# Performance work log

Measured on AMD Instinct MI355X. Metric: run time of the kernel, lower is better.

Reference implementation:

```python
import jax, jax.numpy as jnp
import numpy as np

HIDDEN = 512
HEADS = 8
D_HEAD = HIDDEN // HEADS
SCALE = D_HEAD ** -0.5
LN_EPS = 1e-5
N_L = 2048
N_R = 4096


def setup_inputs() -> dict:
    key = jax.random.key(0)
    ks = jax.random.split(key, 10)
    s = HIDDEN ** -0.5
    return {
        "q": jax.random.normal(ks[0], (N_L, HIDDEN), jnp.float32),
        "kv": jax.random.normal(ks[1], (N_R, HIDDEN), jnp.float32),
        "bias": jax.random.normal(ks[2], (N_L, N_R), jnp.float32),
        "Wq": jax.random.normal(ks[3], (HIDDEN, HIDDEN), jnp.float32) * s,
        "Wk": jax.random.normal(ks[4], (HIDDEN, HIDDEN), jnp.float32) * s,
        "Wv": jax.random.normal(ks[5], (HIDDEN, HIDDEN), jnp.float32) * s,
        "Wo": jax.random.normal(ks[6], (HIDDEN, HIDDEN), jnp.float32) * s,
        "bo": jnp.zeros((HIDDEN,), jnp.float32),
        "gamma": jnp.ones((HIDDEN,), jnp.float32),
        "beta": jnp.zeros((HIDDEN,), jnp.float32),
    }


def reference(q, kv, bias, Wq, Wk, Wv, Wo, bo, gamma, beta):
    # projections (torch Linear: x @ W.T)
    Q = (q @ Wq.T).reshape(N_L, HEADS, D_HEAD).transpose(1, 0, 2)   # [h, N_L, d]
    K = (kv @ Wk.T).reshape(N_R, HEADS, D_HEAD).transpose(1, 0, 2)  # [h, N_R, d]
    V = (kv @ Wv.T).reshape(N_R, HEADS, D_HEAD).transpose(1, 0, 2)  # [h, N_R, d]
    logits = SCALE * jnp.einsum('hld,hrd->hlr', Q, K) + bias[None]  # [h, N_L, N_R]
    attn = jax.nn.softmax(logits, axis=-1)                          # dropout p=0 -> identity
    ctx = jnp.einsum('hlr,hrd->hld', attn, V)                       # [h, N_L, d]
    ctx = ctx.transpose(1, 0, 2).reshape(N_L, HIDDEN)
    out = ctx @ Wo.T + bo
    x = out + q
    mu = jnp.mean(x, axis=-1, keepdims=True)
    var = jnp.mean((x - mu) ** 2, axis=-1, keepdims=True)
    out = (x - mu) * jax.lax.rsqrt(var + LN_EPS) * gamma + beta
    attn_mean = attn.mean(axis=0)                                   # [N_L, N_R]
    return out, attn_mean
```

## Files before the change

kernel.cpp:

```cpp
#include <hip/hip_runtime.h>
#include <hip/hip_bf16.h>
#include <stdint.h>

#define NL 2048
#define NR 4096
#define NCHUNK 8
#define CHUNK (NR / NCHUNK)
#define SCALE 0.125f
#define LN_EPS 1e-5f

typedef __attribute__((ext_vector_type(8))) short short8;
typedef __attribute__((ext_vector_type(4))) float float4v;

static __device__ __forceinline__ short f2bf(float f) {
  union { float f; uint32_t u; } v; v.f = f;
  uint32_t u = v.u;
  uint32_t r = (u + 0x7FFFu + ((u >> 16) & 1u)) >> 16;
  return (short)(r & 0xFFFFu);
}
static __device__ __forceinline__ float bf2f(short b) {
  union { uint32_t u; float f; } v; v.u = ((uint32_t)(uint16_t)b) << 16;
  return v.f;
}

__global__ void k0_cvt(const float* __restrict__ q, const float* __restrict__ kv,
                       const float* __restrict__ Wq, const float* __restrict__ Wk,
                       const float* __restrict__ Wv, const float* __restrict__ Wo,
                       short* __restrict__ qb, short* __restrict__ kvb,
                       short* __restrict__ Wqb, short* __restrict__ Wkb,
                       short* __restrict__ Wvb, short* __restrict__ Wob) {
  int i = blockIdx.x * blockDim.x + threadIdx.x;
  const float* src; short* dst;
  if (i < 131072)                 { src = q;  dst = qb;  }
  else if ((i -= 131072) < 262144){ src = kv; dst = kvb; }
  else if ((i -= 262144) < 32768) { src = Wq; dst = Wqb; }
  else if ((i -= 32768) < 32768)  { src = Wk; dst = Wkb; }
  else if ((i -= 32768) < 32768)  { src = Wv; dst = Wvb; }
  else { i -= 32768;                src = Wo; dst = Wob; }
  const float4* s4 = reinterpret_cast<const float4*>(src) + (size_t)i * 2;
  float4 a = s4[0], b = s4[1];
  short8 o;
  o[0] = f2bf(a.x); o[1] = f2bf(a.y); o[2] = f2bf(a.z); o[3] = f2bf(a.w);
  o[4] = f2bf(b.x); o[5] = f2bf(b.y); o[6] = f2bf(b.z); o[7] = f2bf(b.w);
  *reinterpret_cast<short8*>(dst + (size_t)i * 8) = o;
}

__global__ void k1_proj(const short* __restrict__ qb, const short* __restrict__ kvb,
                        const short* __restrict__ Wqb, const short* __restrict__ Wkb,
                        const short* __restrict__ Wvb,
                        short* __restrict__ Qb, short* __restrict__ Kb,
                        short* __restrict__ VT) {
  int lane = threadIdx.x & 63, warp = threadIdx.x >> 6;
  int wid = blockIdx.x * 4 + warp;
  int lr = lane & 15, lg = lane >> 4;
  const short *src, *W; short* dst; int mt, ct, mode;
  if (wid < 1024)      { src = qb;  W = Wqb; dst = Qb; mt = wid & 127; ct = wid >> 7; mode = 0; }
  else if (wid < 3072) { int id = wid - 1024; src = kvb; W = Wkb; dst = Kb; mt = id & 255; ct = id >> 8; mode = 0; }
  else                 { int id = wid - 3072; src = kvb; W = Wvb; dst = VT; mt = id & 255; ct = id >> 8; mode = 1; }
  int m0 = mt * 16, c0 = ct * 64;
  float4v acc[4] = {};
  const short* arow = src + (m0 + lr) * 512 + 8 * lg;
#pragma unroll
  for (int kk = 0; kk < 16; ++kk) {
    short8 a = *reinterpret_cast<const short8*>(arow + kk * 32);
#pragma unroll
    for (int cs = 0; cs < 4; ++cs) {
      const short* bp = W + (c0 + cs * 16 + lr) * 512 + kk * 32 + 8 * lg;
      short8 b = *reinterpret_cast<const short8*>(bp);
      acc[cs] = __builtin_amdgcn_mfma_f32_16x16x32_bf16(a, b, acc[cs], 0, 0, 0);
    }
  }
  if (mode == 0) {
#pragma unroll
    for (int cs = 0; cs < 4; ++cs)
#pragma unroll
      for (int j = 0; j < 4; ++j)
        dst[(m0 + 4 * lg + j) * 512 + c0 + cs * 16 + lr] = f2bf(acc[cs][j]);
  } else {
#pragma unroll
    for (int cs = 0; cs < 4; ++cs)
#pragma unroll
      for (int j = 0; j < 4; ++j)
        dst[(c0 + cs * 16 + lr) * 4096 + m0 + 4 * lg + j] = f2bf(acc[cs][j]);
  }
}

__global__ void __launch_bounds__(256, 4)
k2_passA(const short* __restrict__ Qb, const short* __restrict__ Kb,
         const float* __restrict__ bias, float* __restrict__ S_part) {
  int lane = threadIdx.x & 63, w = threadIdx.x >> 6;
  int lr = lane & 15, lg = lane >> 4;
  int l0 = blockIdx.x * 16;
  int chunk = blockIdx.y;
  int r_base = chunk * CHUNK;
  float sums[2][4] = {};
  const short* qrow = Qb + (l0 + lr) * 512 + 8 * lg;
  short8 qa[2][2];
#pragma unroll
  for (int hh = 0; hh < 2; ++hh) {
    qa[hh][0] = *reinterpret_cast<const short8*>(qrow + (2 * w + hh) * 64);
    qa[hh][1] = *reinterpret_cast<const short8*>(qrow + (2 * w + hh) * 64 + 32);
  }
#pragma unroll 1
  for (int it = 0; it < CHUNK / 32; ++it) {
    int r0 = r_base + it * 32;
    float bv[2][4];
#pragma unroll
    for (int s = 0; s < 2; ++s)
#pragma unroll
      for (int j = 0; j < 4; ++j)
        bv[s][j] = bias[(l0 + 4 * lg + j) * NR + r0 + s * 16 + lr];
#pragma unroll
    for (int hh = 0; hh < 2; ++hh) {
      int h = 2 * w + hh;
#pragma unroll
      for (int s = 0; s < 2; ++s) {
        const short* kp = Kb + (r0 + s * 16 + lr) * 512 + h * 64 + 8 * lg;
        short8 b0 = *reinterpret_cast<const short8*>(kp);
        short8 b1 = *reinterpret_cast<const short8*>(kp + 32);
        float4v c = {};
        c = __builtin_amdgcn_mfma_f32_16x16x32_bf16(qa[hh][0], b0, c, 0, 0, 0);
        c = __builtin_amdgcn_mfma_f32_16x16x32_bf16(qa[hh][1], b1, c, 0, 0, 0);
#pragma unroll
        for (int j = 0; j < 4; ++j)
          sums[hh][j] += __expf(SCALE * c[j] + bv[s][j]);
      }
    }
  }
#pragma unroll
  for (int hh = 0; hh < 2; ++hh)
#pragma unroll
    for (int j = 0; j < 4; ++j) {
      float v = sums[hh][j];
      v += __shfl_xor(v, 1, 64); v += __shfl_xor(v, 2, 64);
      v += __shfl_xor(v, 4, 64); v += __shfl_xor(v, 8, 64);
      sums[hh][j] = v;
    }
  if (lr == 0) {
#pragma unroll
    for (int hh = 0; hh < 2; ++hh)
#pragma unroll
      for (int j = 0; j < 4; ++j)
        S_part[(chunk * 8 + 2 * w + hh) * NL + l0 + 4 * lg + j] = sums[hh][j];
  }
}

__global__ void k2b_reduceS(const float* __restrict__ S_part, float* __restrict__ Sinv) {
  int i = blockIdx.x * blockDim.x + threadIdx.x;
  int h = i >> 11, l = i & 2047;
  float s = 0.f;
#pragma unroll
  for (int c = 0; c < NCHUNK; ++c) s += S_part[(c * 8 + h) * NL + l];
  Sinv[i] = 1.0f / s;
}

__global__ void __launch_bounds__(256, 4)
k3_passB(const short* __restrict__ Qb, const short* __restrict__ Kb,
         const short* __restrict__ VT, const float* __restrict__ bias,
         const float* __restrict__ Sinv,
         float* __restrict__ attn_mean, short* __restrict__ ctx_part) {
  __shared__ short att[4][16][32];
  __shared__ float maccLDS[4][16][32];
  int lane = threadIdx.x & 63, w = threadIdx.x >> 6;
  int lr = lane & 15, lg = lane >> 4;
  int l0 = blockIdx.x * 16;
  int chunk = blockIdx.y;
  int r_base = chunk * CHUNK;
  float4v acc[8] = {};
  float sinv[2][4];
#pragma unroll
  for (int hh = 0; hh < 2; ++hh)
#pragma unroll
    for (int j = 0; j < 4; ++j)
      sinv[hh][j] = Sinv[(2 * w + hh) * NL + l0 + 4 * lg + j];
  const short* qrow = Qb + (l0 + lr) * 512 + 8 * lg;
  short8 qa[2][2];
#pragma unroll
  for (int hh = 0; hh < 2; ++hh) {
    qa[hh][0] = *reinterpret_cast<const short8*>(qrow + (2 * w + hh) * 64);
    qa[hh][1] = *reinterpret_cast<const short8*>(qrow + (2 * w + hh) * 64 + 32);
  }
  short* myatt = &att[w][0][0];
#pragma unroll 1
  for (int it = 0; it < CHUNK / 32; ++it) {
    int r0 = r_base + it * 32;
    float bv[2][4];
#pragma unroll
    for (int s = 0; s < 2; ++s)
#pragma unroll
      for (int j = 0; j < 4; ++j)
        bv[s][j] = bias[(l0 + 4 * lg + j) * NR + r0 + s * 16 + lr];
    float macc[2][4] = {};
#pragma unroll
    for (int hh = 0; hh < 2; ++hh) {
      int h = 2 * w + hh;
#pragma unroll
      for (int s = 0; s < 2; ++s) {
        const short* kp = Kb + (r0 + s * 16 + lr) * 512 + h * 64 + 8 * lg;
        short8 b0 = *reinterpret_cast<const short8*>(kp);
        short8 b1 = *reinterpret_cast<const short8*>(kp + 32);
        float4v cc = {};
        cc = __builtin_amdgcn_mfma_f32_16x16x32_bf16(qa[hh][0], b0, cc, 0, 0, 0);
        cc = __builtin_amdgcn_mfma_f32_16x16x32_bf16(qa[hh][1], b1, cc, 0, 0, 0);
#pragma unroll
        for (int j = 0; j < 4; ++j) {
          float e = __expf(SCALE * cc[j] + bv[s][j]) * sinv[hh][j];
          macc[s][j] += e;
          myatt[(4 * lg + j) * 32 + s * 16 + lr] = f2bf(e);
        }
      }
      short8 pa = *reinterpret_cast<const short8*>(&att[w][lr][8 * lg]);
#pragma unroll
      for (int ds = 0; ds < 4; ++ds) {
        const short* vp = VT + (h * 64 + ds * 16 + lr) * 4096 + r0 + 8 * lg;
        short8 vb = *reinterpret_cast<const short8*>(vp);
        acc[hh * 4 + ds] = __builtin_amdgcn_mfma_f32_16x16x32_bf16(pa, vb, acc[hh * 4 + ds], 0, 0, 0);
      }
    }
#pragma unroll
    for (int s = 0; s < 2; ++s)
#pragma unroll
      for (int j = 0; j < 4; ++j)
        maccLDS[w][4 * lg + j][s * 16 + lr] = macc[s][j];
    __syncthreads();
    {
      int t = threadIdx.x;
      int row = t >> 4, col = (t & 15) * 2;
      float2 v;
      v.x = (maccLDS[0][row][col] + maccLDS[1][row][col] +
             maccLDS[2][row][col] + maccLDS[3][row][col]) * 0.125f;
      v.y = (maccLDS[0][row][col + 1] + maccLDS[1][row][col + 1] +
             maccLDS[2][row][col + 1] + maccLDS[3][row][col + 1]) * 0.125f;
      *reinterpret_cast<float2*>(&attn_mean[(size_t)(l0 + row) * NR + r0 + col]) = v;
    }
    __syncthreads();
  }
#pragma unroll
  for (int hh = 0; hh < 2; ++hh)
#pragma unroll
    for (int ds = 0; ds < 4; ++ds)
#pragma unroll
      for (int j = 0; j < 4; ++j)
        ctx_part[(chunk * NL + l0 + 4 * lg + j) * 512 + (2 * w + hh) * 64 + ds * 16 + lr] =
            f2bf(acc[hh * 4 + ds][j]);
}

__global__ void k4pre(const short* __restrict__ ctx_part, short* __restrict__ ctxsum) {
  int i = blockIdx.x * blockDim.x + threadIdx.x;
  float sm[8] = {};
#pragma unroll
  for (int c = 0; c < NCHUNK; ++c) {
    short8 v = *reinterpret_cast<const short8*>(ctx_part + (size_t)c * NL * 512 + (size_t)i * 8);
#pragma unroll
    for (int u = 0; u < 8; ++u) sm[u] += bf2f(v[u]);
  }
  short8 o;
#pragma unroll
  for (int u = 0; u < 8; ++u) o[u] = f2bf(sm[u]);
  *reinterpret_cast<short8*>(ctxsum + (size_t)i * 8) = o;
}

__global__ void k4_out(const short* __restrict__ ctxsum, const short* __restrict__ Wob,
                       const float* __restrict__ q, const float* __restrict__ bo,
                       const float* __restrict__ gamma, const float* __restrict__ beta,
                       float* __restrict__ out) {
  __shared__ float xs[16][512];
  int lane = threadIdx.x & 63, warp = threadIdx.x >> 6;
  int lr = lane & 15, lg = lane >> 4;
  int l0 = blockIdx.x * 16;
  short8 afr[16];
#pragma unroll
  for (int kk = 0; kk < 16; ++kk)
    afr[kk] = *reinterpret_cast<const short8*>(ctxsum + (l0 + lr) * 512 + kk * 32 + 8 * lg);
#pragma unroll 1
  for (int cs = 0; cs < 8; ++cs) {
    int col0 = warp * 128 + cs * 16;
    float4v c = {};
#pragma unroll
    for (int kk = 0; kk < 16; ++kk) {
      const short* bp = Wob + (col0 + lr) * 512 + kk * 32 + 8 * lg;
      short8 b = *reinterpret_cast<const short8*>(bp);
      c = __builtin_amdgcn_mfma_f32_16x16x32_bf16(afr[kk], b, c, 0, 0, 0);
    }
#pragma unroll
    for (int j = 0; j < 4; ++j) {
      int row = l0 + 4 * lg + j, col = col0 + lr;
      xs[4 * lg + j][col] = c[j] + bo[col] + q[row * 512 + col];
    }
  }
  __syncthreads();
  int tid = threadIdx.x;
  int rl = tid >> 4, g = tid & 15;
  float sum = 0.f;
#pragma unroll
  for (int i = 0; i < 32; ++i) sum += xs[rl][g + 16 * i];
  sum += __shfl_xor(sum, 1, 64); sum += __shfl_xor(sum, 2, 64);
  sum += __shfl_xor(sum, 4, 64); sum += __shfl_xor(sum, 8, 64);
  float mu = sum * (1.0f / 512.0f);
  float vs = 0.f;
#pragma unroll
  for (int i = 0; i < 32; ++i) { float d = xs[rl][g + 16 * i] - mu; vs += d * d; }
  vs += __shfl_xor(vs, 1, 64); vs += __shfl_xor(vs, 2, 64);
  vs += __shfl_xor(vs, 4, 64); vs += __shfl_xor(vs, 8, 64);
  float rs = rsqrtf(vs * (1.0f / 512.0f) + LN_EPS);
#pragma unroll
  for (int i = 0; i < 32; ++i) {
    int cc = g + 16 * i;
    out[(l0 + rl) * 512 + cc] = (xs[rl][cc] - mu) * rs * gamma[cc] + beta[cc];
  }
}

extern "C" void kernel_launch(void* const* d_in, const int* in_sizes, int n_in,
                              void* d_out, int out_size, void* d_ws, size_t ws_size,
                              hipStream_t stream) {
  const float* q     = (const float*)d_in[0];
  const float* kv    = (const float*)d_in[1];
  const float* bias  = (const float*)d_in[2];
  const float* Wq    = (const float*)d_in[3];
  const float* Wk    = (const float*)d_in[4];
  const float* Wv    = (const float*)d_in[5];
  const float* Wo    = (const float*)d_in[6];
  const float* bo    = (const float*)d_in[7];
  const float* gamma = (const float*)d_in[8];
  const float* beta  = (const float*)d_in[9];
  float* out = (float*)d_out;
  float* attn_mean = out + (size_t)NL * 512;

  char* ws = (char*)d_ws;
  short* qb       = (short*)(ws + 0);
  short* kvb      = (short*)(ws + 2097152);
  short* Wqb      = (short*)(ws + 6291456);
  short* Wkb      = (short*)(ws + 6815744);
  short* Wvb      = (short*)(ws + 7340032);
  short* Wob      = (short*)(ws + 7864320);
  short* Qb       = (short*)(ws + 8388608);
  short* Kb       = (short*)(ws + 10485760);
  short* VT       = (short*)(ws + 14680064);
  float* S_part   = (float*)(ws + 18874368);
  float* Sinv     = (float*)(ws + 19398656);
  short* ctx_part = (short*)(ws + 19464192);
  short* ctxsum   = (short*)(ws + 36241408);

  k0_cvt<<<2048, 256, 0, stream>>>(q, kv, Wq, Wk, Wv, Wo, qb, kvb, Wqb, Wkb, Wvb, Wob);
  k1_proj<<<1280, 256, 0, stream>>>(qb, kvb, Wqb, Wkb, Wvb, Qb, Kb, VT);
  k2_passA<<<dim3(128, 8), 256, 0, stream>>>(Qb, Kb, bias, S_part);
  k2b_reduceS<<<64, 256, 0, stream>>>(S_part, Sinv);
  k3_passB<<<dim3(128, 8), 256, 0, stream>>>(Qb, Kb, VT, bias, Sinv, attn_mean, ctx_part);
  k4pre<<<512, 256, 0, stream>>>(ctx_part, ctxsum);
  k4_out<<<128, 256, 0, stream>>>(ctxsum, Wob, q, bo, gamma, beta, out);
}
```

Before: 379.0 us.

## Assign one wave per head in attention passes with 512-thread blocks

```diff
diff --git a/kernel.cpp b/kernel.cpp
--- a/kernel.cpp
+++ b/kernel.cpp
@@ -85,7 +85,7 @@
   }
 }
 
-__global__ void __launch_bounds__(256, 4)
+__global__ void __launch_bounds__(512, 8)
 k2_passA(const short* __restrict__ Qb, const short* __restrict__ Kb,
          const float* __restrict__ bias, float* __restrict__ S_part) {
   int lane = threadIdx.x & 63, w = threadIdx.x >> 6;
@@ -93,14 +93,10 @@
   int l0 = blockIdx.x * 16;
   int chunk = blockIdx.y;
   int r_base = chunk * CHUNK;
-  float sums[2][4] = {};
+  float sums[4] = {};
   const short* qrow = Qb + (l0 + lr) * 512 + 8 * lg;
-  short8 qa[2][2];
-#pragma unroll
-  for (int hh = 0; hh < 2; ++hh) {
-    qa[hh][0] = *reinterpret_cast<const short8*>(qrow + (2 * w + hh) * 64);
-    qa[hh][1] = *reinterpret_cast<const short8*>(qrow + (2 * w + hh) * 64 + 32);
-  }
+  short8 qa0 = *reinterpret_cast<const short8*>(qrow + w * 64);
+  short8 qa1 = *reinterpret_cast<const short8*>(qrow + w * 64 + 32);
 #pragma unroll 1
   for (int it = 0; it < CHUNK / 32; ++it) {
     int r0 = r_base + it * 32;
@@ -110,38 +106,34 @@
 #pragma unroll
       for (int j = 0; j < 4; ++j)
         bv[s][j] = bias[(l0 + 4 * lg + j) * NR + r0 + s * 16 + lr];
-#pragma unroll
-    for (int hh = 0; hh < 2; ++hh) {
-      int h = 2 * w + hh;
-#pragma unroll
-      for (int s = 0; s < 2; ++s) {
-        const short* kp = Kb + (r0 + s * 16 + lr) * 512 + h * 64 + 8 * lg;
-        short8 b0 = *reinterpret_cast<const short8*>(kp);
-        short8 b1 = *reinterpret_cast<const short8*>(kp + 32);
-        float4v c = {};
-        c = __builtin_amdgcn_mfma_f32_16x16x32_bf16(qa[hh][0], b0, c, 0, 0, 0);
-        c = __builtin_amdgcn_mfma_f32_16x16x32_bf16(qa[hh][1], b1, c, 0, 0, 0);
-#pragma unroll
-        for (int j = 0; j < 4; ++j)
-          sums[hh][j] += __expf(SCALE * c[j] + bv[s][j]);
-      }
-    }
-  }
-#pragma unroll
-  for (int hh = 0; hh < 2; ++hh)
-#pragma unroll
-    for (int j = 0; j < 4; ++j) {
-      float v = sums[hh][j];
-      v += __shfl_xor(v, 1, 64); v += __shfl_xor(v, 2, 64);
-      v += __shfl_xor(v, 4, 64); v += __shfl_xor(v, 8, 64);
-      sums[hh][j] = v;
-    }
+    float4v cc[2];
+#pragma unroll
+    for (int s = 0; s < 2; ++s) {
+      const short* kp = Kb + (r0 + s * 16 + lr) * 512 + w * 64 + 8 * lg;
+      short8 b0 = *reinterpret_cast<const short8*>(kp);
+      short8 b1 = *reinterpret_cast<const short8*>(kp + 32);
+      float4v c = {};
+      c = __builtin_amdgcn_mfma_f32_16x16x32_bf16(qa0, b0, c, 0, 0, 0);
+      c = __builtin_amdgcn_mfma_f32_16x16x32_bf16(qa1, b1, c, 0, 0, 0);
+      cc[s] = c;
+    }
+#pragma unroll
+    for (int s = 0; s < 2; ++s)
+#pragma unroll
+      for (int j = 0; j < 4; ++j)
+        sums[j] += __expf(SCALE * cc[s][j] + bv[s][j]);
+  }
+#pragma unroll
+  for (int j = 0; j < 4; ++j) {
+    float v = sums[j];
+    v += __shfl_xor(v, 1, 64); v += __shfl_xor(v, 2, 64);
+    v += __shfl_xor(v, 4, 64); v += __shfl_xor(v, 8, 64);
+    sums[j] = v;
+  }
   if (lr == 0) {
 #pragma unroll
-    for (int hh = 0; hh < 2; ++hh)
-#pragma unroll
-      for (int j = 0; j < 4; ++j)
-        S_part[(chunk * 8 + 2 * w + hh) * NL + l0 + 4 * lg + j] = sums[hh][j];
+    for (int j = 0; j < 4; ++j)
+      S_part[(chunk * 8 + w) * NL + l0 + 4 * lg + j] = sums[j];
   }
 }
 
@@ -154,32 +146,26 @@
   Sinv[i] = 1.0f / s;
 }
 
-__global__ void __launch_bounds__(256, 4)
+__global__ void __launch_bounds__(512, 8)
 k3_passB(const short* __restrict__ Qb, const short* __restrict__ Kb,
          const short* __restrict__ VT, const float* __restrict__ bias,
          const float* __restrict__ Sinv,
          float* __restrict__ attn_mean, short* __restrict__ ctx_part) {
-  __shared__ short att[4][16][32];
-  __shared__ float maccLDS[4][16][32];
+  __shared__ __align__(16) short att[8][16][32];
+  __shared__ float maccLDS[8][16][32];
   int lane = threadIdx.x & 63, w = threadIdx.x >> 6;
   int lr = lane & 15, lg = lane >> 4;
   int l0 = blockIdx.x * 16;
   int chunk = blockIdx.y;
   int r_base = chunk * CHUNK;
-  float4v acc[8] = {};
-  float sinv[2][4];
-#pragma unroll
-  for (int hh = 0; hh < 2; ++hh)
-#pragma unroll
-    for (int j = 0; j < 4; ++j)
-      sinv[hh][j] = Sinv[(2 * w + hh) * NL + l0 + 4 * lg + j];
+  float4v acc[4] = {};
+  float sinv[4];
+#pragma unroll
+  for (int j = 0; j < 4; ++j)
+    sinv[j] = Sinv[w * NL + l0 + 4 * lg + j];
   const short* qrow = Qb + (l0 + lr) * 512 + 8 * lg;
-  short8 qa[2][2];
-#pragma unroll
-  for (int hh = 0; hh < 2; ++hh) {
-    qa[hh][0] = *reinterpret_cast<const short8*>(qrow + (2 * w + hh) * 64);
-    qa[hh][1] = *reinterpret_cast<const short8*>(qrow + (2 * w + hh) * 64 + 32);
-  }
+  short8 qa0 = *reinterpret_cast<const short8*>(qrow + w * 64);
+  short8 qa1 = *reinterpret_cast<const short8*>(qrow + w * 64 + 32);
   short* myatt = &att[w][0][0];
 #pragma unroll 1
   for (int it = 0; it < CHUNK / 32; ++it) {
@@ -190,59 +176,55 @@
 #pragma unroll
       for (int j = 0; j < 4; ++j)
         bv[s][j] = bias[(l0 + 4 * lg + j) * NR + r0 + s * 16 + lr];
-    float macc[2][4] = {};
-#pragma unroll
-    for (int hh = 0; hh < 2; ++hh) {
-      int h = 2 * w + hh;
-#pragma unroll
-      for (int s = 0; s < 2; ++s) {
-        const short* kp = Kb + (r0 + s * 16 + lr) * 512 + h * 64 + 8 * lg;
-        short8 b0 = *reinterpret_cast<const short8*>(kp);
-        short8 b1 = *reinterpret_cast<const short8*>(kp + 32);
-        float4v cc = {};
-        cc = __builtin_amdgcn_mfma_f32_16x16x32_bf16(qa[hh][0], b0, cc, 0, 0, 0);
-        cc = __builtin_amdgcn_mfma_f32_16x16x32_bf16(qa[hh][1], b1, cc, 0, 0, 0);
-#pragma unroll
-        for (int j = 0; j < 4; ++j) {
-          float e = __expf(SCALE * cc[j] + bv[s][j]) * sinv[hh][j];
-          macc[s][j] += e;
-          myatt[(4 * lg + j) * 32 + s * 16 + lr] = f2bf(e);
-        }
+    float4v cc[2];
+#pragma unroll
+    for (int s = 0; s < 2; ++s) {
+      const short* kp = Kb + (r0 + s * 16 + lr) * 512 + w * 64 + 8 * lg;
+      short8 b0 = *reinterpret_cast<const short8*>(kp);
+      short8 b1 = *reinterpret_cast<const short8*>(kp + 32);
+      float4v c = {};
+      c = __builtin_amdgcn_mfma_f32_16x16x32_bf16(qa0, b0, c, 0, 0, 0);
+      c = __builtin_amdgcn_mfma_f32_16x16x32_bf16(qa1, b1, c, 0, 0, 0);
+      cc[s] = c;
+    }
+    float macc[2][4];
+#pragma unroll
+    for (int s = 0; s < 2; ++s)
+#pragma unroll
+      for (int j = 0; j < 4; ++j) {
+        float e = __expf(SCALE * cc[s][j] + bv[s][j]);
+        macc[s][j] = e;
+        myatt[(4 * lg + j) * 32 + s * 16 + lr] = f2bf(e);
       }
-      short8 pa = *reinterpret_cast<const short8*>(&att[w][lr][8 * lg]);
-#pragma unroll
-      for (int ds = 0; ds < 4; ++ds) {
-        const short* vp = VT + (h * 64 + ds * 16 + lr) * 4096 + r0 + 8 * lg;
-        short8 vb = *reinterpret_cast<const short8*>(vp);
-        acc[hh * 4 + ds] = __builtin_amdgcn_mfma_f32_16x16x32_bf16(pa, vb, acc[hh * 4 + ds], 0, 0, 0);
-      }
-    }
-#pragma unroll
-    for (int s = 0; s < 2; ++s)
-#pragma unroll
-      for (int j = 0; j < 4; ++j)
-        maccLDS[w][4 * lg + j][s * 16 + lr] = macc[s][j];
+    short8 pa = *reinterpret_cast<const short8*>(&att[w][lr][8 * lg]);
+#pragma unroll
+    for (int ds = 0; ds < 4; ++ds) {
+      const short* vp = VT + (w * 64 + ds * 16 + lr) * 4096 + r0 + 8 * lg;
+      short8 vb = *reinterpret_cast<const short8*>(vp);
+      acc[ds] = __builtin_amdgcn_mfma_f32_16x16x32_bf16(pa, vb, acc[ds], 0, 0, 0);
+    }
+#pragma unroll
+    for (int s = 0; s < 2; ++s)
+#pragma unroll
+      for (int j = 0; j < 4; ++j)
+        maccLDS[w][4 * lg + j][s * 16 + lr] = macc[s][j] * sinv[j];
     __syncthreads();
     {
       int t = threadIdx.x;
-      int row = t >> 4, col = (t & 15) * 2;
-      float2 v;
-      v.x = (maccLDS[0][row][col] + maccLDS[1][row][col] +
-             maccLDS[2][row][col] + maccLDS[3][row][col]) * 0.125f;
-      v.y = (maccLDS[0][row][col + 1] + maccLDS[1][row][col + 1] +
-             maccLDS[2][row][col + 1] + maccLDS[3][row][col + 1]) * 0.125f;
-      *reinterpret_cast<float2*>(&attn_mean[(size_t)(l0 + row) * NR + r0 + col]) = v;
+      int row = t >> 5, col = t & 31;
+      float v = 0.f;
+#pragma unroll
+      for (int hh = 0; hh < 8; ++hh) v += maccLDS[hh][row][col];
+      attn_mean[(size_t)(l0 + row) * NR + r0 + col] = v * 0.125f;
     }
     __syncthreads();
   }
 #pragma unroll
-  for (int hh = 0; hh < 2; ++hh)
-#pragma unroll
-    for (int ds = 0; ds < 4; ++ds)
-#pragma unroll
-      for (int j = 0; j < 4; ++j)
-        ctx_part[(chunk * NL + l0 + 4 * lg + j) * 512 + (2 * w + hh) * 64 + ds * 16 + lr] =
-            f2bf(acc[hh * 4 + ds][j]);
+  for (int ds = 0; ds < 4; ++ds)
+#pragma unroll
+    for (int j = 0; j < 4; ++j)
+      ctx_part[(chunk * NL + l0 + 4 * lg + j) * 512 + w * 64 + ds * 16 + lr] =
+          f2bf(acc[ds][j] * sinv[j]);
 }
 
 __global__ void k4pre(const short* __restrict__ ctx_part, short* __restrict__ ctxsum) {
@@ -343,9 +325,9 @@
 
   k0_cvt<<<2048, 256, 0, stream>>>(q, kv, Wq, Wk, Wv, Wo, qb, kvb, Wqb, Wkb, Wvb, Wob);
   k1_proj<<<1280, 256, 0, stream>>>(qb, kvb, Wqb, Wkb, Wvb, Qb, Kb, VT);
-  k2_passA<<<dim3(128, 8), 256, 0, stream>>>(Qb, Kb, bias, S_part);
+  k2_passA<<<dim3(128, 8), 512, 0, stream>>>(Qb, Kb, bias, S_part);
   k2b_reduceS<<<64, 256, 0, stream>>>(S_part, Sinv);
-  k3_passB<<<dim3(128, 8), 256, 0, stream>>>(Qb, Kb, VT, bias, Sinv, attn_mean, ctx_part);
+  k3_passB<<<dim3(128, 8), 512, 0, stream>>>(Qb, Kb, VT, bias, Sinv, attn_mean, ctx_part);
   k4pre<<<512, 256, 0, stream>>>(ctx_part, ctxsum);
   k4_out<<<128, 256, 0, stream>>>(ctxsum, Wob, q, bo, gamma, beta, out);
 }
```

Result: no change. 374.0 us (-1.3%).
